# Kernel optimization log

Measured on AMD Instinct MI355X. Metric: run time of the kernel, lower is better.

## Reference

```python
import jax, jax.numpy as jnp
import numpy as np

N_NODES = 50000
N_EDGES = 400000
IN_DIM = 512
OUT_DIM = 512


def setup_inputs() -> dict:
    key = jax.random.key(0)
    k1, k2, k3, k4 = jax.random.split(key, 4)
    x = jax.random.normal(k1, (N_NODES, IN_DIM), dtype=jnp.float32)
    edge_index = jax.random.randint(k2, (2, N_EDGES), 0, N_NODES, dtype=jnp.int64)
    # nn.Linear(in_dim, out_dim): weight [out, in], bias [out]
    W = jax.random.normal(k3, (OUT_DIM, IN_DIM), dtype=jnp.float32) / np.sqrt(IN_DIM)
    b = jax.random.normal(k4, (OUT_DIM,), dtype=jnp.float32) * 0.01
    return {"x": x, "edge_index": edge_index, "W": W, "b": b}


def reference(x, edge_index, W, b):
    n = x.shape[0]
    loops = jnp.arange(n, dtype=edge_index.dtype)
    row = jnp.concatenate([edge_index[0], loops])  # src
    col = jnp.concatenate([edge_index[1], loops])  # dst
    # degree from row counts (matches torch.bincount(row)); self-loops ensure deg >= 1
    deg = jax.ops.segment_sum(jnp.ones(row.shape[0], dtype=x.dtype), row, num_segments=n)
    dis = jax.lax.rsqrt(deg)  # deg^-0.5
    norm = dis[row] * dis[col]  # [E+N]
    h = x @ W.T + b  # [N, out_dim]
    # out[dst] += norm * h[src], fused gather-scale-scatter
    out = jax.ops.segment_sum(norm[:, None] * h[row], col, num_segments=n)
    return jax.nn.relu(out)
```

## Files before the change

kernel.cpp:

```cpp
#include <hip/hip_runtime.h>
#include <hip/hip_bf16.h>

#define K_DIM 512
#define N_DIM 512

typedef __attribute__((ext_vector_type(8))) short s8v;
typedef __attribute__((ext_vector_type(4))) short s4v;
typedef __attribute__((ext_vector_type(4))) float f4v;

__device__ __forceinline__ short f2bf(float f) {
  union { float f; unsigned u; } v; v.f = f;
  unsigned r = (v.u + 0x7FFFu + ((v.u >> 16) & 1u)) >> 16;
  return (short)r;
}
__device__ __forceinline__ float bflo(unsigned u) {
  union { unsigned u; float f; } v; v.u = u << 16; return v.f;
}
__device__ __forceinline__ float bfhi(unsigned u) {
  union { unsigned u; float f; } v; v.u = u & 0xffff0000u; return v.f;
}

__device__ __forceinline__ void gload16(const void* g, void* l) {
  __builtin_amdgcn_global_load_lds(
      (const __attribute__((address_space(1))) void*)g,
      (__attribute__((address_space(3))) void*)l, 16, 0, 0);
}

__device__ __forceinline__ int edge_stride(const int* __restrict__ e32, int lane) {
  int chk = e32[2 * lane + 1];
  unsigned long long m = __ballot(chk == 0);
  return (m == ~0ULL) ? 2 : 1;
}

__global__ __launch_bounds__(256) void k_pre1(const float* __restrict__ W,
    short* __restrict__ Wb, const float* __restrict__ x, short* __restrict__ xs,
    long long n4 , const int* __restrict__ e32,
    int* __restrict__ outdeg, int* __restrict__ indeg, int E, int nbw, int nbx) {
  int b = blockIdx.x;
  int t = threadIdx.x;
  if (b < nbw) {
    int i = (b * 256 + t) * 4;
    float4 f = *(const float4*)(W + i);
    s4v s; s[0] = f2bf(f.x); s[1] = f2bf(f.y); s[2] = f2bf(f.z); s[3] = f2bf(f.w);
    *(s4v*)(Wb + i) = s;
  } else if (b < nbw + nbx) {
    const float4* x4 = (const float4*)x;
    s4v* xs4 = (s4v*)xs;
    long long i0 = (long long)(b - nbw) * 256 + t;
    const long long stride = (long long)nbx * 256;
    for (long long i = i0; i < n4; i += 4 * stride) {
      float4 f[4];
      #pragma unroll
      for (int u = 0; u < 4; ++u) {
        long long j = i + u * stride;
        f[u] = (j < n4) ? x4[j] : float4{0.f, 0.f, 0.f, 0.f};
      }
      #pragma unroll
      for (int u = 0; u < 4; ++u) {
        long long j = i + u * stride;
        if (j < n4) {
          s4v s;
          s[0] = f2bf(f[u].x); s[1] = f2bf(f[u].y);
          s[2] = f2bf(f[u].z); s[3] = f2bf(f[u].w);
          xs4[j] = s;
        }
      }
    }
  } else {
    int st = edge_stride(e32, t & 63);
    int i = (b - nbw - nbx) * 256 + t;
    if (i < E) {
      int r = e32[(size_t)i * st];
      int c = e32[(size_t)(E + i) * st];
      atomicAdd(&outdeg[r], 1);
      atomicAdd(&indeg[c], 1);
    }
  }
}

__global__ __launch_bounds__(256) void k_pre2(const int* __restrict__ outdeg,
    float* __restrict__ dis, const int* __restrict__ indeg, int* __restrict__ part,
    int n, int nbd) {
  int b = blockIdx.x;
  if (b < nbd) {
    int i = b * 256 + threadIdx.x;
    if (i < n) dis[i] = rsqrtf((float)(outdeg[i] + 1));
  } else {
    __shared__ int sm[256];
    int lb = b - nbd;
    int i = lb * 256 + threadIdx.x;
    sm[threadIdx.x] = (i < n) ? indeg[i] : 0;
    __syncthreads();
    for (int off = 128; off > 0; off >>= 1) {
      if (threadIdx.x < off) sm[threadIdx.x] += sm[threadIdx.x + off];
      __syncthreads();
    }
    if (threadIdx.x == 0) part[lb] = sm[0];
  }
}

__global__ __launch_bounds__(256) void k_scan(const int* __restrict__ indeg,
    const int* __restrict__ part, int* __restrict__ row_start,
    int* __restrict__ cursor, int n, int nb) {
  __shared__ int sp[256];
  __shared__ int sm[256];
  int t = threadIdx.x, b = blockIdx.x;
  sp[t] = (t < nb) ? part[t] : 0;
  __syncthreads();
  for (int off = 1; off < 256; off <<= 1) {
    int a = (t >= off) ? sp[t - off] : 0;
    __syncthreads();
    sp[t] += a;
    __syncthreads();
  }
  int pOff = (b > 0) ? sp[b - 1] : 0;
  if (b == 0 && t == 255) row_start[n] = sp[255];
  int i = b * 256 + t;
  int v = (i < n) ? indeg[i] : 0;
  sm[t] = v;
  __syncthreads();
  for (int off = 1; off < 256; off <<= 1) {
    int a = (t >= off) ? sm[t - off] : 0;
    __syncthreads();
    sm[t] += a;
    __syncthreads();
  }
  if (i < n) {
    int excl = pOff + sm[t] - v;
    row_start[i] = excl;
    cursor[i] = excl;
  }
}

__global__ __launch_bounds__(256) void k_fill(const int* __restrict__ e32,
    int* __restrict__ cursor, int* __restrict__ csr, int E) {
  int st = edge_stride(e32, threadIdx.x & 63);
  int i = blockIdx.x * blockDim.x + threadIdx.x;
  if (i >= E) return;
  int r = e32[(size_t)i * st];
  int c = e32[(size_t)(E + i) * st];
  int p = atomicAdd(&cursor[c], 1);
  csr[p] = r;
}

__device__ __forceinline__ void fma4(float* acc, uint2 rv, float w) {
  acc[0] += w * bflo(rv.x); acc[1] += w * bfhi(rv.x);
  acc[2] += w * bflo(rv.y); acc[3] += w * bfhi(rv.y);
}

__global__ __launch_bounds__(256) void k_agg(const short* __restrict__ xs,
    const float* __restrict__ dis, const int* __restrict__ row_start,
    const int* __restrict__ csr, short* __restrict__ xa, float* __restrict__ s,
    int n, int coff, int writeS) {
  int wid = blockIdx.x * 4 + (threadIdx.x >> 6);
  int nw = gridDim.x * 4;
  int lane = threadIdx.x & 63;
  const short* hl = xs + coff + lane * 4;
  for (int v = wid; v < n; v += nw) {
    float dv = dis[v];
    float acc[4];
    float accs = dv;
    {
      uint2 r = *(const uint2*)(hl + (size_t)v * N_DIM);
      acc[0] = dv * bflo(r.x); acc[1] = dv * bfhi(r.x);
      acc[2] = dv * bflo(r.y); acc[3] = dv * bfhi(r.y);
    }
    int sb = __builtin_amdgcn_readfirstlane(row_start[v]);
    int eb = __builtin_amdgcn_readfirstlane(row_start[v + 1]);
    int idx = sb;
    for (; idx + 8 <= eb; idx += 8) {
      int s0 = csr[idx],     s1 = csr[idx + 1], s2 = csr[idx + 2], s3 = csr[idx + 3];
      int s4 = csr[idx + 4], s5 = csr[idx + 5], s6 = csr[idx + 6], s7 = csr[idx + 7];
      float w0 = dis[s0], w1 = dis[s1], w2 = dis[s2], w3 = dis[s3];
      float w4 = dis[s4], w5 = dis[s5], w6 = dis[s6], w7 = dis[s7];
      uint2 r0 = *(const uint2*)(hl + (size_t)s0 * N_DIM);
      uint2 r1 = *(const uint2*)(hl + (size_t)s1 * N_DIM);
      uint2 r2 = *(const uint2*)(hl + (size_t)s2 * N_DIM);
      uint2 r3 = *(const uint2*)(hl + (size_t)s3 * N_DIM);
      uint2 r4 = *(const uint2*)(hl + (size_t)s4 * N_DIM);
      uint2 r5 = *(const uint2*)(hl + (size_t)s5 * N_DIM);
      uint2 r6 = *(const uint2*)(hl + (size_t)s6 * N_DIM);
      uint2 r7 = *(const uint2*)(hl + (size_t)s7 * N_DIM);
      accs += w0 + w1 + w2 + w3 + w4 + w5 + w6 + w7;
      fma4(acc, r0, w0); fma4(acc, r1, w1); fma4(acc, r2, w2); fma4(acc, r3, w3);
      fma4(acc, r4, w4); fma4(acc, r5, w5); fma4(acc, r6, w6); fma4(acc, r7, w7);
    }
    for (; idx + 4 <= eb; idx += 4) {
      int s0 = csr[idx], s1 = csr[idx + 1], s2 = csr[idx + 2], s3 = csr[idx + 3];
      float w0 = dis[s0], w1 = dis[s1], w2 = dis[s2], w3 = dis[s3];
      uint2 r0 = *(const uint2*)(hl + (size_t)s0 * N_DIM);
      uint2 r1 = *(const uint2*)(hl + (size_t)s1 * N_DIM);
      uint2 r2 = *(const uint2*)(hl + (size_t)s2 * N_DIM);
      uint2 r3 = *(const uint2*)(hl + (size_t)s3 * N_DIM);
      accs += w0 + w1 + w2 + w3;
      fma4(acc, r0, w0); fma4(acc, r1, w1); fma4(acc, r2, w2); fma4(acc, r3, w3);
    }
    for (; idx < eb; ++idx) {
      int s0 = csr[idx];
      float w0 = dis[s0];
      uint2 r0 = *(const uint2*)(hl + (size_t)s0 * N_DIM);
      accs += w0;
      fma4(acc, r0, w0);
    }
    s4v o;
    o[0] = f2bf(dv * acc[0]); o[1] = f2bf(dv * acc[1]);
    o[2] = f2bf(dv * acc[2]); o[3] = f2bf(dv * acc[3]);
    *(s4v*)(xa + (size_t)v * N_DIM + coff + lane * 4) = o;
    if (writeS && lane == 0) s[v] = dv * accs;
  }
}

__global__ __launch_bounds__(256, 4) void k_gemm(const short* __restrict__ xa,
    const short* __restrict__ Wb, const float* __restrict__ bias,
    const float* __restrict__ s, float* __restrict__ out, int M) {
  __shared__ __align__(16) char smem[32768];
  short* As = (short*)smem;
  short* Bs = (short*)(smem + 16384);
  int nwg = gridDim.x;
  int orig = blockIdx.x;
  int q8 = nwg >> 3, r8 = nwg & 7;
  int xcd = orig & 7, pos = orig >> 3;
  int swz = (xcd < r8 ? xcd * (q8 + 1) : r8 * (q8 + 1) + (xcd - r8) * q8) + pos;
  const int n0 = (swz & 3) * 128;
  const int m0 = (swz >> 2) * 128;

  const int tid = threadIdx.x;
  const int lane = tid & 63;
  const int wv = tid >> 6, wr = wv >> 1, wc = wv & 1;
  const int la = lane & 15, lg = lane >> 4;

  const short* ag[2];
  const short* bg[2];
  int doff[2];
  #pragma unroll
  for (int r = 0; r < 2; ++r) {
    int id = r * 256 + tid;
    int row = id >> 2;
    int ch = id & 3;
    int arow = m0 + row; if (arow >= M) arow = M - 1;
    ag[r] = xa + (size_t)arow * K_DIM + ch * 8;
    bg[r] = Wb + (size_t)(n0 + row) * K_DIM + ch * 8;
    doff[r] = (r * 256 + (tid & 192)) * 16;
  }
  int aro[4], bro[4];
  #pragma unroll
  for (int i = 0; i < 4; ++i) {
    aro[i] = (64 * wr + 16 * i + la) * 64 + lg * 16;
    bro[i] = (64 * wc + 16 * i + la) * 64 + lg * 16;
  }

  f4v acc[4][4] = {};

  #pragma unroll
  for (int r = 0; r < 2; ++r) {
    gload16(ag[r], (char*)As + doff[r]);
    gload16(bg[r], (char*)Bs + doff[r]);
  }
  __syncthreads();

  for (int kt = 0; kt < 16; ++kt) {
    const int cur = kt & 1;
    const int nxt = cur ^ 1;
    if (kt < 15) {
      const int kk = (kt + 1) * 32;
      #pragma unroll
      for (int r = 0; r < 2; ++r) {
        gload16(ag[r] + kk, (char*)As + nxt * 8192 + doff[r]);
        gload16(bg[r] + kk, (char*)Bs + nxt * 8192 + doff[r]);
      }
    }
    s8v af[4], bf[4];
    const char* ab = (const char*)As + cur * 8192;
    const char* bb = (const char*)Bs + cur * 8192;
    #pragma unroll
    for (int i = 0; i < 4; ++i) af[i] = *(const s8v*)(ab + aro[i]);
    #pragma unroll
    for (int j = 0; j < 4; ++j) bf[j] = *(const s8v*)(bb + bro[j]);
    #pragma unroll
    for (int i = 0; i < 4; ++i)
      #pragma unroll
      for (int j = 0; j < 4; ++j)
        acc[i][j] = __builtin_amdgcn_mfma_f32_16x16x32_bf16(af[i], bf[j], acc[i][j], 0, 0, 0);
    __syncthreads();
  }

  float* Es = (float*)(smem + wv * 4352);
  float bv[4];
  #pragma unroll
  for (int j = 0; j < 4; ++j) bv[j] = bias[n0 + 64 * wc + 16 * j + la];
  #pragma unroll
  for (int i = 0; i < 4; ++i) {
    int rowb = m0 + 64 * wr + 16 * i + lg * 4;
    float sv[4];
    #pragma unroll
    for (int r = 0; r < 4; ++r) sv[r] = (rowb + r < M) ? s[rowb + r] : 0.f;
    #pragma unroll
    for (int j = 0; j < 4; ++j)
      #pragma unroll
      for (int r = 0; r < 4; ++r)
        Es[(lg * 4 + r) * 68 + 16 * j + la] = fmaxf(acc[i][j][r] + sv[r] * bv[j], 0.f);
    asm volatile("s_waitcnt lgkmcnt(0)" ::: "memory");
    int gr0 = m0 + 64 * wr + 16 * i;
    #pragma unroll
    for (int rr = 0; rr < 4; ++rr) {
      int id = rr * 64 + lane;
      int rl = id >> 4, ch = id & 15;
      f4v val = *(const f4v*)&Es[rl * 68 + ch * 4];
      if (gr0 + rl < M)
        __builtin_nontemporal_store(val,
            (f4v*)(out + (size_t)(gr0 + rl) * N_DIM + n0 + 64 * wc + ch * 4));
    }
    asm volatile("s_waitcnt lgkmcnt(0)" ::: "memory");
  }
}

extern "C" void kernel_launch(void* const* d_in, const int* in_sizes, int n_in,
                              void* d_out, int out_size, void* d_ws, size_t ws_size,
                              hipStream_t stream) {
  const float* x = (const float*)d_in[0];
  const int* e32 = (const int*)d_in[1];
  const float* W = (const float*)d_in[2];
  const float* bias = (const float*)d_in[3];
  float* out = (float*)d_out;
  int M = in_sizes[0] / K_DIM;
  int E = in_sizes[1] / 2;

  char* ws = (char*)d_ws;
  size_t off = 0;
  auto alloc = [&](size_t bytes) {
    void* p = ws + off;
    off = (off + bytes + 255) & ~(size_t)255;
    return p;
  };
  short* Wb      = (short*)alloc((size_t)N_DIM * K_DIM * 2);
  short* xa      = (short*)alloc((size_t)M * N_DIM * 2);
  float* dis     = (float*)alloc((size_t)M * 4);
  float* sv      = (float*)alloc((size_t)M * 4);
  int*   outdeg  = (int*)alloc((size_t)M * 4);
  int*   indeg   = (int*)alloc((size_t)M * 4);
  int*   rstart  = (int*)alloc((size_t)(M + 1) * 4);
  int*   cursor  = (int*)alloc((size_t)M * 4);
  int*   part    = (int*)alloc(256 * 4);
  int*   csr     = (int*)alloc((size_t)E * 4);
  if (off > ws_size) return;

  short* xs = (short*)d_out;

  size_t zbytes = (size_t)((char*)indeg - (char*)outdeg) + (size_t)M * 4;
  (void)hipMemsetAsync(outdeg, 0, zbytes, stream);

  long long n4 = (long long)M * K_DIM / 4;
  int nbw = N_DIM * K_DIM / 4 / 256;
  int nbx = 2048;
  int nbh = (E + 255) / 256;
  k_pre1<<<nbw + nbx + nbh, 256, 0, stream>>>(W, Wb, x, xs, n4, e32,
                                              outdeg, indeg, E, nbw, nbx);
  int nscan = (M + 255) / 256;
  k_pre2<<<nscan * 2, 256, 0, stream>>>(outdeg, dis, indeg, part, M, nscan);
  k_scan<<<nscan, 256, 0, stream>>>(indeg, part, rstart, cursor, M, nscan);
  k_fill<<<nbh, 256, 0, stream>>>(e32, cursor, csr, E);
  k_agg<<<2048, 256, 0, stream>>>(xs, dis, rstart, csr, xa, sv, M, 0, 1);
  k_agg<<<2048, 256, 0, stream>>>(xs, dis, rstart, csr, xa, sv, M, 256, 0);
  int nmc = (M + 127) / 128;
  k_gemm<<<nmc * 4, 256, 0, stream>>>(xa, Wb, bias, sv, out, M);
}
```

Before: 199.1 us.

## Privatize degree histograms into 8 copies and move x conversion into fill kernel

Degree counting now spreads its atomics over 8 privatized counters per node, chosen by block and thread group, and later kernels sum the 8 copies. This is meant to reduce same-address atomic contention. The x fp32-to-bf16 conversion moves from the first kernel to the CSR fill kernel, so the bandwidth-heavy conversion overlaps with the atomic-bound fill instead of the histogram. In exchange, the counters grow 8x, which adds memset and readback traffic.

```diff
diff --git a/kernel.cpp b/kernel.cpp
--- a/kernel.cpp
+++ b/kernel.cpp
@@ -32,10 +32,9 @@
   return (m == ~0ULL) ? 2 : 1;
 }
 
-__global__ __launch_bounds__(256) void k_pre1(const float* __restrict__ W,
-    short* __restrict__ Wb, const float* __restrict__ x, short* __restrict__ xs,
-    long long n4 , const int* __restrict__ e32,
-    int* __restrict__ outdeg, int* __restrict__ indeg, int E, int nbw, int nbx) {
+__global__ __launch_bounds__(256) void k_histW(const float* __restrict__ W,
+    short* __restrict__ Wb, const int* __restrict__ e32,
+    int* __restrict__ outdeg8, int* __restrict__ indeg8, int E, int nbw) {
   int b = blockIdx.x;
   int t = threadIdx.x;
   if (b < nbw) {
@@ -43,11 +42,99 @@
     float4 f = *(const float4*)(W + i);
     s4v s; s[0] = f2bf(f.x); s[1] = f2bf(f.y); s[2] = f2bf(f.z); s[3] = f2bf(f.w);
     *(s4v*)(Wb + i) = s;
-  } else if (b < nbw + nbx) {
+  } else {
+    int st = edge_stride(e32, t & 63);
+    int i = (b - nbw) * 256 + t;
+    if (i < E) {
+      int r = e32[(size_t)i * st];
+      int c = e32[(size_t)(E + i) * st];
+      int cp = (b + (t >> 3)) & 7;
+      atomicAdd(&outdeg8[r * 8 + cp], 1);
+      atomicAdd(&indeg8[c * 8 + cp], 1);
+    }
+  }
+}
+
+__device__ __forceinline__ int sum8(const int* __restrict__ p) {
+  int4 a = *(const int4*)p;
+  int4 b = *(const int4*)(p + 4);
+  return a.x + a.y + a.z + a.w + b.x + b.y + b.z + b.w;
+}
+
+__global__ __launch_bounds__(256) void k_pre2(const int* __restrict__ outdeg8,
+    float* __restrict__ dis, const int* __restrict__ indeg8, int* __restrict__ part,
+    int n, int nbd) {
+  int b = blockIdx.x;
+  if (b < nbd) {
+    int i = b * 256 + threadIdx.x;
+    if (i < n) dis[i] = rsqrtf((float)(sum8(outdeg8 + i * 8) + 1));
+  } else {
+    __shared__ int sm[256];
+    int lb = b - nbd;
+    int i = lb * 256 + threadIdx.x;
+    sm[threadIdx.x] = (i < n) ? sum8(indeg8 + i * 8) : 0;
+    __syncthreads();
+    for (int off = 128; off > 0; off >>= 1) {
+      if (threadIdx.x < off) sm[threadIdx.x] += sm[threadIdx.x + off];
+      __syncthreads();
+    }
+    if (threadIdx.x == 0) part[lb] = sm[0];
+  }
+}
+
+__global__ __launch_bounds__(256) void k_scan(const int* __restrict__ indeg8,
+    const int* __restrict__ part, int* __restrict__ row_start,
+    int* __restrict__ cursor, int n, int nb) {
+  __shared__ int sp[256];
+  __shared__ int sm[256];
+  int t = threadIdx.x, b = blockIdx.x;
+  sp[t] = (t < nb) ? part[t] : 0;
+  __syncthreads();
+  for (int off = 1; off < 256; off <<= 1) {
+    int a = (t >= off) ? sp[t - off] : 0;
+    __syncthreads();
+    sp[t] += a;
+    __syncthreads();
+  }
+  int pOff = (b > 0) ? sp[b - 1] : 0;
+  if (b == 0 && t == 255) row_start[n] = sp[255];
+  int i = b * 256 + t;
+  int v = (i < n) ? sum8(indeg8 + i * 8) : 0;
+  sm[t] = v;
+  __syncthreads();
+  for (int off = 1; off < 256; off <<= 1) {
+    int a = (t >= off) ? sm[t - off] : 0;
+    __syncthreads();
+    sm[t] += a;
+    __syncthreads();
+  }
+  if (i < n) {
+    int excl = pOff + sm[t] - v;
+    row_start[i] = excl;
+    cursor[i] = excl;
+  }
+}
+
+__global__ __launch_bounds__(256) void k_fillconv(const int* __restrict__ e32,
+    int* __restrict__ cursor, int* __restrict__ csr, int E,
+    const float* __restrict__ x, short* __restrict__ xs, long long n4,
+    int nbh, int nbc) {
+  int b = blockIdx.x;
+  int t = threadIdx.x;
+  if (b < nbh) {
+    int st = edge_stride(e32, t & 63);
+    int i = b * 256 + t;
+    if (i < E) {
+      int r = e32[(size_t)i * st];
+      int c = e32[(size_t)(E + i) * st];
+      int p = atomicAdd(&cursor[c], 1);
+      csr[p] = r;
+    }
+  } else {
     const float4* x4 = (const float4*)x;
     s4v* xs4 = (s4v*)xs;
-    long long i0 = (long long)(b - nbw) * 256 + t;
-    const long long stride = (long long)nbx * 256;
+    long long i0 = (long long)(b - nbh) * 256 + t;
+    const long long stride = (long long)nbc * 256;
     for (long long i = i0; i < n4; i += 4 * stride) {
       float4 f[4];
       #pragma unroll
@@ -66,81 +153,7 @@
         }
       }
     }
-  } else {
-    int st = edge_stride(e32, t & 63);
-    int i = (b - nbw - nbx) * 256 + t;
-    if (i < E) {
-      int r = e32[(size_t)i * st];
-      int c = e32[(size_t)(E + i) * st];
-      atomicAdd(&outdeg[r], 1);
-      atomicAdd(&indeg[c], 1);
-    }
-  }
-}
-
-__global__ __launch_bounds__(256) void k_pre2(const int* __restrict__ outdeg,
-    float* __restrict__ dis, const int* __restrict__ indeg, int* __restrict__ part,
-    int n, int nbd) {
-  int b = blockIdx.x;
-  if (b < nbd) {
-    int i = b * 256 + threadIdx.x;
-    if (i < n) dis[i] = rsqrtf((float)(outdeg[i] + 1));
-  } else {
-    __shared__ int sm[256];
-    int lb = b - nbd;
-    int i = lb * 256 + threadIdx.x;
-    sm[threadIdx.x] = (i < n) ? indeg[i] : 0;
-    __syncthreads();
-    for (int off = 128; off > 0; off >>= 1) {
-      if (threadIdx.x < off) sm[threadIdx.x] += sm[threadIdx.x + off];
-      __syncthreads();
-    }
-    if (threadIdx.x == 0) part[lb] = sm[0];
-  }
-}
-
-__global__ __launch_bounds__(256) void k_scan(const int* __restrict__ indeg,
-    const int* __restrict__ part, int* __restrict__ row_start,
-    int* __restrict__ cursor, int n, int nb) {
-  __shared__ int sp[256];
-  __shared__ int sm[256];
-  int t = threadIdx.x, b = blockIdx.x;
-  sp[t] = (t < nb) ? part[t] : 0;
-  __syncthreads();
-  for (int off = 1; off < 256; off <<= 1) {
-    int a = (t >= off) ? sp[t - off] : 0;
-    __syncthreads();
-    sp[t] += a;
-    __syncthreads();
-  }
-  int pOff = (b > 0) ? sp[b - 1] : 0;
-  if (b == 0 && t == 255) row_start[n] = sp[255];
-  int i = b * 256 + t;
-  int v = (i < n) ? indeg[i] : 0;
-  sm[t] = v;
-  __syncthreads();
-  for (int off = 1; off < 256; off <<= 1) {
-    int a = (t >= off) ? sm[t - off] : 0;
-    __syncthreads();
-    sm[t] += a;
-    __syncthreads();
-  }
-  if (i < n) {
-    int excl = pOff + sm[t] - v;
-    row_start[i] = excl;
-    cursor[i] = excl;
-  }
-}
-
-__global__ __launch_bounds__(256) void k_fill(const int* __restrict__ e32,
-    int* __restrict__ cursor, int* __restrict__ csr, int E) {
-  int st = edge_stride(e32, threadIdx.x & 63);
-  int i = blockIdx.x * blockDim.x + threadIdx.x;
-  if (i >= E) return;
-  int r = e32[(size_t)i * st];
-  int c = e32[(size_t)(E + i) * st];
-  int p = atomicAdd(&cursor[c], 1);
-  csr[p] = r;
+  }
 }
 
 __device__ __forceinline__ void fma4(float* acc, uint2 rv, float w) {
@@ -336,8 +349,8 @@
   short* xa      = (short*)alloc((size_t)M * N_DIM * 2);
   float* dis     = (float*)alloc((size_t)M * 4);
   float* sv      = (float*)alloc((size_t)M * 4);
-  int*   outdeg  = (int*)alloc((size_t)M * 4);
-  int*   indeg   = (int*)alloc((size_t)M * 4);
+  int*   outdeg8 = (int*)alloc((size_t)M * 32);
+  int*   indeg8  = (int*)alloc((size_t)M * 32);
   int*   rstart  = (int*)alloc((size_t)(M + 1) * 4);
   int*   cursor  = (int*)alloc((size_t)M * 4);
   int*   part    = (int*)alloc(256 * 4);
@@ -346,19 +359,18 @@
 
   short* xs = (short*)d_out;
 
-  size_t zbytes = (size_t)((char*)indeg - (char*)outdeg) + (size_t)M * 4;
-  (void)hipMemsetAsync(outdeg, 0, zbytes, stream);
+  size_t zbytes = (size_t)((char*)indeg8 - (char*)outdeg8) + (size_t)M * 32;
+  (void)hipMemsetAsync(outdeg8, 0, zbytes, stream);
 
   long long n4 = (long long)M * K_DIM / 4;
   int nbw = N_DIM * K_DIM / 4 / 256;
-  int nbx = 2048;
   int nbh = (E + 255) / 256;
-  k_pre1<<<nbw + nbx + nbh, 256, 0, stream>>>(W, Wb, x, xs, n4, e32,
-                                              outdeg, indeg, E, nbw, nbx);
+  int nbc = 2048;
+  k_histW<<<nbw + nbh, 256, 0, stream>>>(W, Wb, e32, outdeg8, indeg8, E, nbw);
   int nscan = (M + 255) / 256;
-  k_pre2<<<nscan * 2, 256, 0, stream>>>(outdeg, dis, indeg, part, M, nscan);
-  k_scan<<<nscan, 256, 0, stream>>>(indeg, part, rstart, cursor, M, nscan);
-  k_fill<<<nbh, 256, 0, stream>>>(e32, cursor, csr, E);
+  k_pre2<<<nscan * 2, 256, 0, stream>>>(outdeg8, dis, indeg8, part, M, nscan);
+  k_scan<<<nscan, 256, 0, stream>>>(indeg8, part, rstart, cursor, M, nscan);
+  k_fillconv<<<nbh + nbc, 256, 0, stream>>>(e32, cursor, csr, E, x, xs, n4, nbh, nbc);
   k_agg<<<2048, 256, 0, stream>>>(xs, dis, rstart, csr, xa, sv, M, 0, 1);
   k_agg<<<2048, 256, 0, stream>>>(xs, dis, rstart, csr, xa, sv, M, 256, 0);
   int nmc = (M + 127) / 128;
```

Measured after the change: 206.0 us. +3.4%, slower.
